# Kernel optimization log

Measured on AMD Instinct MI355X. Metric: run time of the kernel, lower is better.

Reference implementation:

```python
import jax, jax.numpy as jnp
import numpy as np

# --- constants matching DILConfig ---
N_DIFF = 1000      # num_diffusion_steps
STEPS = 4          # inference_steps
S_MAX = 4          # max_scales
BUDGET = 0.2       # entropy_budget
G0 = 2.0           # guidance_strength
ENT_LO = 0.1       # stability_threshold_low
ENT_HI = 0.5       # stability_threshold_high
B, L, C, H = 16, 1024, 128, 512


def setup_inputs() -> dict:
    key = jax.random.key(0)
    ks = jax.random.split(key, 6)
    y_obs = jax.random.normal(ks[0], (B, L, C), dtype=jnp.float32)
    mask = (jax.random.uniform(ks[1], (B, L, C)) > 0.5).astype(jnp.float32)
    z_init = jax.random.normal(ks[2], (B, L, C), dtype=jnp.float32)
    W1 = jax.random.normal(ks[3], (C, H), dtype=jnp.float32) / np.sqrt(C)
    b1 = jnp.zeros((H,), dtype=jnp.float32)
    W2 = jax.random.normal(ks[4], (H, C), dtype=jnp.float32) / np.sqrt(H)
    b2 = jnp.zeros((C,), dtype=jnp.float32)
    tw = jax.random.normal(ks[5], (H,), dtype=jnp.float32)
    return {"y_obs": y_obs, "mask": mask, "z_init": z_init,
            "W1": W1, "b1": b1, "W2": W2, "b2": b2, "tw": tw}


def _dil_forward(y_obs, mask, z_init, W1, b1, W2, b2, tw):
    # diffusion schedule (linear betas)
    betas = jnp.linspace(1e-4, 0.02, N_DIFF, dtype=jnp.float32)
    ac = jnp.cumprod(1.0 - betas)
    alpha = jnp.sqrt(ac)                     # sqrt_alphas_cumprod
    sigma = jnp.sqrt(1.0 - ac)               # sqrt_one_minus_alphas_cumprod
    lam = jnp.log(alpha) - jnp.log(sigma)    # log-SNR/2

    step = N_DIFF // STEPS
    ks = [N_DIFF - 1 - i * step for i in range(STEPS)]

    def score(z, k):
        # epsilon predictor: channel MLP with scalar time feature
        t_feat = jnp.float32(k) / N_DIFF
        h = jax.nn.gelu(jnp.einsum('blc,ch->blh', z, W1) + b1 + t_feat * tw)
        return jnp.einsum('blh,hc->blc', h, W2) + b2

    z = z_init
    for k in ks:  # fixed small unrolled loop over inference steps
        kp = max(k - step, 0)
        eps = score(z, k)                                   # [B,L,C]
        h_lam = lam[kp] - lam[k]
        base_a = alpha[kp] / alpha[k]
        base_b = sigma[kp] * (jnp.exp(h_lam) - 1.0)

        # entropy map: batch-mean |eps| per pixel
        ent_pix = jnp.mean(jnp.abs(eps), axis=0)            # [L,C]

        # self-guidance on observed entries
        obs_err = (z - y_obs) * mask
        guidance = -obs_err / (jnp.var(obs_err) + 1e-8)     # [B,L,C]

        z_new = z
        # coarse -> fine so finer-scale selected nodes overwrite coarser ones
        for s in range(S_MAX - 1, -1, -1):
            w = 2 ** s
            pooled = ent_pix.reshape(L // w, w, C // w, w).mean(axis=(1, 3))
            Knodes = max(1, int(BUDGET * pooled.size))
            _, idx = jax.lax.top_k(pooled.ravel(), Knodes)
            selg = jnp.zeros((pooled.size,), jnp.float32).at[idx].set(1.0)
            selg = selg.reshape(pooled.shape)
            sel = jnp.repeat(jnp.repeat(selg, w, axis=0), w, axis=1)     # [L,C]
            ent_up = jnp.repeat(jnp.repeat(pooled, w, axis=0), w, axis=1)

            # adaptive solver order from entropy stability thresholds
            order = (1.0 + (ent_up > ENT_LO).astype(jnp.float32)
                         + (ent_up > ENT_HI).astype(jnp.float32))
            corr = (1.0 + (order - 1.0) * 0.5 * h_lam
                        + (order - 1.0) * (order - 2.0) / 6.0 * h_lam ** 2)
            gs = G0 * ent_up / (ent_up + 1.0)               # adaptive guidance

            cand = base_a * z - base_b * (corr * eps) + gs * guidance
            z_new = jnp.where(sel[None, :, :] > 0, cand, z_new)
        z = z_new
    return z


def reference(y_obs, mask, z_init, W1, b1, W2, b2, tw):
    return _dil_forward(y_obs, mask, z_init, W1, b1, W2, b2, tw)
```

## Files before the change

kernel.cpp:

```cpp
#include <hip/hip_runtime.h>
#include <math.h>
#include <stdint.h>

#define L_DIM 1024
#define C_DIM 128
#define H_DIM 512
#define B_DIM 16
#define LC (L_DIM * C_DIM)
#define BLC (B_DIM * LC)

typedef __attribute__((ext_vector_type(8))) short short8;
typedef __attribute__((ext_vector_type(4))) float floatx4;

__device__ __forceinline__ unsigned fordbits(unsigned u) {
    return (u & 0x80000000u) ? ~u : (u | 0x80000000u);
}

__device__ __forceinline__ void split3(float x, unsigned& uh, unsigned& um,
                                       unsigned& ul) {
    uh = __float_as_uint(x);
    const float r1 = x - __uint_as_float(uh & 0xffff0000u);
    um = __float_as_uint(r1);
    const float r2 = r1 - __uint_as_float(um & 0xffff0000u);
    ul = __float_as_uint(r2);
}

__device__ __forceinline__ float gelu_fast(float x) {
    const float g = 0.7978845608028654f * (x + 0.044715f * x * x * x);
    const float e = __expf(2.0f * g);
    const float t = 1.0f - 2.0f / (e + 1.0f);
    return 0.5f * x * (1.0f + t);
}

__global__ __launch_bounds__(256) void wsplit_kernel(
    const float* __restrict__ W1, const float* __restrict__ W2,
    unsigned short* __restrict__ W1h, unsigned short* __restrict__ W1m,
    unsigned short* __restrict__ W1l, unsigned short* __restrict__ W2h,
    unsigned short* __restrict__ W2m, unsigned short* __restrict__ W2l,
    unsigned* __restrict__ zeroblk) {
    const int t = blockIdx.x * 256 + threadIdx.x;
    if (t < 16396) zeroblk[t] = 0u;
    unsigned uh, um, ul;
    if (t < 65536) {
        const int j = t & 7, lane = (t >> 3) & 63, nt = (t >> 9) & 31,
                  kt = (t >> 14) & 3;
        const int k = kt * 32 + (lane >> 4) * 8 + j;
        const int n = nt * 16 + (lane & 15);
        split3(W1[k * 512 + n], uh, um, ul);
        W1h[t] = (unsigned short)(uh >> 16);
        W1m[t] = (unsigned short)(um >> 16);
        W1l[t] = (unsigned short)(ul >> 16);
    } else {
        const int t2 = t - 65536;
        const int j = t2 & 7, lane = (t2 >> 3) & 63, nt = (t2 >> 9) & 7,
                  kt = (t2 >> 12) & 15;
        const int k = kt * 32 + (lane >> 4) * 8 + j;
        const int n = nt * 16 + (lane & 15);
        split3(W2[k * 128 + n], uh, um, ul);
        W2h[t2] = (unsigned short)(uh >> 16);
        W2m[t2] = (unsigned short)(um >> 16);
        W2l[t2] = (unsigned short)(ul >> 16);
    }
}

#define MFMA6(AH, AM, AL, BH, BM, BL, ACC)                                    \
    ACC = __builtin_amdgcn_mfma_f32_16x16x32_bf16(AL, BH, ACC, 0, 0, 0);      \
    ACC = __builtin_amdgcn_mfma_f32_16x16x32_bf16(AM, BM, ACC, 0, 0, 0);      \
    ACC = __builtin_amdgcn_mfma_f32_16x16x32_bf16(AH, BL, ACC, 0, 0, 0);      \
    ACC = __builtin_amdgcn_mfma_f32_16x16x32_bf16(AM, BH, ACC, 0, 0, 0);      \
    ACC = __builtin_amdgcn_mfma_f32_16x16x32_bf16(AH, BM, ACC, 0, 0, 0);      \
    ACC = __builtin_amdgcn_mfma_f32_16x16x32_bf16(AH, BH, ACC, 0, 0, 0);

__device__ __forceinline__ int swz(int row, int col) {
    return row * 128 + ((((col >> 3) ^ (row & 15))) << 3) + (col & 7);
}

template <int UPD>
__global__ __launch_bounds__(512, 2) void mlp_kernel(
    float* __restrict__ z, const float* __restrict__ zr,
    const float* __restrict__ y, const float* __restrict__ mk,
    const unsigned short* __restrict__ W1h, const unsigned short* __restrict__ W1m,
    const unsigned short* __restrict__ W1l, const unsigned short* __restrict__ W2h,
    const unsigned short* __restrict__ W2m, const unsigned short* __restrict__ W2l,
    const float* __restrict__ b1, const float* __restrict__ tw,
    const float* __restrict__ b2, float t_feat,
    float* __restrict__ eps_buf, float* __restrict__ ent,
    const float* __restrict__ cA, const float* __restrict__ cB,
    const float* __restrict__ cG, float* __restrict__ accum,
    float* __restrict__ p1, float* __restrict__ p2,
    unsigned* __restrict__ ghist) {
    __shared__ unsigned short zA[3][8192];
    __shared__ unsigned short hA[3][8192];
    __shared__ float entbuf[4][128];
    __shared__ float red1[8], red2[8];
    const int tid = threadIdx.x;
    const int w = tid >> 6, lane = tid & 63;
    const int quad = lane >> 4, m16 = lane & 15;
    const int l0 = blockIdx.x * 4;

    float s1 = 0.f, s2 = 0.f;
#pragma unroll
    for (int e = 0; e < 4; ++e) {
        const int f = (e * 512 + tid) * 4;
        const int r_ = f >> 7, cb = f & 127;
        const int b = r_ & 15, il = r_ >> 4, l = l0 + il;
        const size_t g = ((size_t)b * 1024 + l) * 128 + cb;
        float4 zv = *(const float4*)(zr + g);
        const float4 yv = *(const float4*)(y + g);
        const float4 mv = *(const float4*)(mk + g);
        if (UPD) {
            const float4 ev = *(const float4*)(eps_buf + g);
            const int pix = l * 128 + cb;
            const float4 a4 = *(const float4*)(cA + pix);
            const float4 b4 = *(const float4*)(cB + pix);
            const float4 g4 = *(const float4*)(cG + pix);
            zv.x = a4.x * zv.x - b4.x * ev.x - g4.x * ((zv.x - yv.x) * mv.x);
            zv.y = a4.y * zv.y - b4.y * ev.y - g4.y * ((zv.y - yv.y) * mv.y);
            zv.z = a4.z * zv.z - b4.z * ev.z - g4.z * ((zv.z - yv.z) * mv.z);
            zv.w = a4.w * zv.w - b4.w * ev.w - g4.w * ((zv.w - yv.w) * mv.w);
            *(float4*)(z + g) = zv;
        }
        float oe;
        oe = (zv.x - yv.x) * mv.x; s1 += oe; s2 += oe * oe;
        oe = (zv.y - yv.y) * mv.y; s1 += oe; s2 += oe * oe;
        oe = (zv.z - yv.z) * mv.z; s1 += oe; s2 += oe * oe;
        oe = (zv.w - yv.w) * mv.w; s1 += oe; s2 += oe * oe;

        const int base = swz(r_, cb);
        const float xs[4] = {zv.x, zv.y, zv.z, zv.w};
        ushort4 vh, vm, vl;
        unsigned uh, um, ul;
        split3(xs[0], uh, um, ul); vh.x = uh >> 16; vm.x = um >> 16; vl.x = ul >> 16;
        split3(xs[1], uh, um, ul); vh.y = uh >> 16; vm.y = um >> 16; vl.y = ul >> 16;
        split3(xs[2], uh, um, ul); vh.z = uh >> 16; vm.z = um >> 16; vl.z = ul >> 16;
        split3(xs[3], uh, um, ul); vh.w = uh >> 16; vm.w = um >> 16; vl.w = ul >> 16;
        *(ushort4*)(&zA[0][base]) = vh;
        *(ushort4*)(&zA[1][base]) = vm;
        *(ushort4*)(&zA[2][base]) = vl;
    }
#pragma unroll
    for (int off = 32; off; off >>= 1) {
        s1 += __shfl_down(s1, off);
        s2 += __shfl_down(s2, off);
    }
    if (lane == 0) { red1[w] = s1; red2[w] = s2; }
    __syncthreads();
    if (tid == 0) {
        float a1 = 0.f, a2 = 0.f;
#pragma unroll
        for (int i = 0; i < 8; ++i) { a1 += red1[i]; a2 += red2[i]; }
        atomicAdd(&accum[0], a1);
        atomicAdd(&accum[1], a2);
    }

    floatx4 acc1[16];
#pragma unroll
    for (int i = 0; i < 16; ++i) acc1[i] = (floatx4){0.f, 0.f, 0.f, 0.f};

#pragma unroll
    for (int kt = 0; kt < 4; ++kt) {
        short8 Ah[4], Am[4], Al[4];
#pragma unroll
        for (int il = 0; il < 4; ++il) {
            const int fb = swz(il * 16 + m16, kt * 32 + quad * 8);
            Ah[il] = *(const short8*)(&zA[0][fb]);
            Am[il] = *(const short8*)(&zA[1][fb]);
            Al[il] = *(const short8*)(&zA[2][fb]);
        }
#pragma unroll
        for (int q = 0; q < 4; ++q) {
            const size_t off = ((size_t)(kt * 32 + q * 8 + w) * 64 + lane) * 8;
            const short8 bh = *(const short8*)(W1h + off);
            const short8 bm = *(const short8*)(W1m + off);
            const short8 bl = *(const short8*)(W1l + off);
#pragma unroll
            for (int il = 0; il < 4; ++il) {
                floatx4 a = acc1[q * 4 + il];
                MFMA6(Ah[il], Am[il], Al[il], bh, bm, bl, a);
                acc1[q * 4 + il] = a;
            }
        }
    }

    floatx4 acc2[4];
#pragma unroll
    for (int i = 0; i < 4; ++i) acc2[i] = (floatx4){0.f, 0.f, 0.f, 0.f};

#pragma unroll
    for (int q = 0; q < 4; ++q) {
        {
            const int colg = q * 128 + w * 16 + m16;
            const float bb = b1[colg] + t_feat * tw[colg];
            const int kcol = w * 16 + m16;
#pragma unroll
            for (int il = 0; il < 4; ++il) {
#pragma unroll
                for (int r = 0; r < 4; ++r) {
                    const float x = gelu_fast(acc1[q * 4 + il][r] + bb);
                    unsigned uh, um, ul;
                    split3(x, uh, um, ul);
                    const int idx = swz(il * 16 + quad * 4 + r, kcol);
                    hA[0][idx] = (unsigned short)(uh >> 16);
                    hA[1][idx] = (unsigned short)(um >> 16);
                    hA[2][idx] = (unsigned short)(ul >> 16);
                }
            }
        }
        __syncthreads();

#pragma unroll
        for (int ktl = 0; ktl < 4; ++ktl) {
            short8 Ah2[4], Am2[4], Al2[4];
#pragma unroll
            for (int il = 0; il < 4; ++il) {
                const int fb = swz(il * 16 + m16, ktl * 32 + quad * 8);
                Ah2[il] = *(const short8*)(&hA[0][fb]);
                Am2[il] = *(const short8*)(&hA[1][fb]);
                Al2[il] = *(const short8*)(&hA[2][fb]);
            }
            const size_t off =
                ((size_t)((q * 4 + ktl) * 8 + w) * 64 + lane) * 8;
            const short8 bh = *(const short8*)(W2h + off);
            const short8 bm = *(const short8*)(W2m + off);
            const short8 bl = *(const short8*)(W2l + off);
#pragma unroll
            for (int il = 0; il < 4; ++il) {
                floatx4 a = acc2[il];
                MFMA6(Ah2[il], Am2[il], Al2[il], bh, bm, bl, a);
                acc2[il] = a;
            }
        }
        __syncthreads();
    }

    {
        const int col = w * 16 + m16;
        const float bb2 = b2[col];
#pragma unroll
        for (int il = 0; il < 4; ++il) {
            float pa = 0.f;
#pragma unroll
            for (int r = 0; r < 4; ++r) {
                const float e = acc2[il][r] + bb2;
                const int b = quad * 4 + r;
                eps_buf[((size_t)b * 1024 + l0 + il) * 128 + col] = e;
                pa += fabsf(e);
            }
            pa += __shfl_xor(pa, 16);
            pa += __shfl_xor(pa, 32);
            if (quad == 0) {
                const float ev = pa * (1.0f / 16.0f);
                ent[(l0 + il) * 128 + col] = ev;
                entbuf[il][col] = ev;
            }
        }
    }

    unsigned* lhist = (unsigned*)&hA[0][0];
    for (int i = tid; i < 8192; i += 512) lhist[i] = 0u;
    __syncthreads();
    if (tid < 512) {
        const float v = entbuf[tid >> 7][tid & 127];
        const unsigned b = fordbits(__float_as_uint(v)) >> 18;
        atomicAdd(&lhist[b >> 1], 1u << ((b & 1) << 4));
    }
    if (tid < 128) {
        const int ir = tid >> 6, c = tid & 63;
        float s = entbuf[2 * ir][2 * c];
        s += entbuf[2 * ir][2 * c + 1];
        s += entbuf[2 * ir + 1][2 * c];
        s += entbuf[2 * ir + 1][2 * c + 1];
        p1[(2 * (int)blockIdx.x + ir) * 64 + c] = s * 0.25f;
    }
    if (tid < 32) {
        const int c = tid;
        float s = 0.f;
#pragma unroll
        for (int ii = 0; ii < 4; ++ii) {
            s += entbuf[ii][4 * c];
            s += entbuf[ii][4 * c + 1];
            s += entbuf[ii][4 * c + 2];
            s += entbuf[ii][4 * c + 3];
        }
        p2[(int)blockIdx.x * 32 + c] = s * 0.0625f;
    }
    __syncthreads();
    for (int i = tid; i < 8192; i += 512) {
        const unsigned v = lhist[i];
        if (v & 0xFFFFu) atomicAdd(&ghist[2 * i], v & 0xFFFFu);
        if (v >> 16) atomicAdd(&ghist[2 * i + 1], v >> 16);
    }
}


__device__ __forceinline__ void suffix_scan_block(unsigned* __restrict__ part,
                                                  unsigned* __restrict__ wtot,
                                                  const int n, const int t) {
    const int lane = t & 63, w = t >> 6;
    const int nw = n >> 6;
    unsigned s = (t < n) ? part[t] : 0u;
#pragma unroll
    for (int off = 1; off < 64; off <<= 1) {
        const unsigned v = __shfl_down(s, off);
        if (lane + off < 64) s += v;
    }
    if (t < n && lane == 0) wtot[w] = s;
    __syncthreads();
    if (t < n) {
        unsigned o = 0;
        for (int j = w + 1; j < nw; ++j) o += wtot[j];
        part[t] = s + o;
    }
    __syncthreads();
}

#define CAND_CAP 16384

__device__ __forceinline__ void wave_compact(bool pred, unsigned val,
                                             unsigned* __restrict__ sh_cnt,
                                             unsigned* __restrict__ buf,
                                             const int lane) {
    const unsigned long long mask = __ballot(pred);
    if (mask == 0ull) return;
    unsigned base = 0u;
    if (lane == 0)
        base = atomicAdd(sh_cnt, (unsigned)__popcll(mask));
    base = __shfl(base, 0);
    if (pred) {
        const unsigned rank =
            (unsigned)__popcll(mask & ((1ull << lane) - 1ull));
        const unsigned p = base + rank;
        if (p < CAND_CAP) buf[p] = val;
    }
}

template <int NPT4, int N, unsigned K>
__device__ __forceinline__ void small_select_vals(
    const float4* xv, unsigned* __restrict__ gout, const int t,
    const int w8, unsigned* __restrict__ histcand,
    unsigned* __restrict__ part, unsigned (*hrep)[512],
    unsigned* __restrict__ wtot,
    unsigned* sh_b, unsigned* sh_krem, unsigned* sh_cnt, unsigned* sh_d,
    unsigned* sh_k2) {
    const int lane = t & 63;
    unsigned u[NPT4 * 4];
#pragma unroll
    for (int i = 0; i < NPT4; ++i) {
        u[4 * i + 0] = fordbits(__float_as_uint(xv[i].x));
        u[4 * i + 1] = fordbits(__float_as_uint(xv[i].y));
        u[4 * i + 2] = fordbits(__float_as_uint(xv[i].z));
        u[4 * i + 3] = fordbits(__float_as_uint(xv[i].w));
    }
    if (t == 0) { *sh_b = 0u; *sh_krem = 1u; *sh_cnt = 0u; *sh_d = 0u; *sh_k2 = 1u; }
    for (int i = t; i < 16384; i += 1024) histcand[i] = 0u;
    __syncthreads();
#pragma unroll
    for (int j = 0; j < NPT4 * 4; ++j) atomicAdd(&histcand[u[j] >> 18], 1u);
    __syncthreads();
    {
        unsigned s = 0;
#pragma unroll
        for (int j = 0; j < 16; ++j) s += histcand[t * 16 + j];
        part[t] = s;
    }
    suffix_scan_block(part, wtot, 1024, t);
    {
        const unsigned suf = part[t];
        const unsigned sufn = (t < 1023) ? part[t + 1] : 0u;
        if (suf >= K && sufn < K) {
            unsigned run = sufn;
            for (int b = 15; b >= 0; --b) {
                const unsigned hb = histcand[t * 16 + b];
                run += hb;
                if (run >= K) {
                    *sh_b = (unsigned)(t * 16 + b);
                    *sh_krem = K - (run - hb);
                    break;
                }
            }
        }
    }
    __syncthreads();
    const unsigned b14 = *sh_b;
    unsigned krem = *sh_krem;
    __syncthreads();
#pragma unroll
    for (int j = 0; j < NPT4 * 4; ++j)
        wave_compact((u[j] >> 18) == b14, u[j], sh_cnt, histcand, lane);
    __syncthreads();
    const unsigned cnt = *sh_cnt;
    const bool inlds = (cnt <= CAND_CAP);
    for (int i = t; i < 4096; i += 1024) ((unsigned*)hrep)[i] = 0u;
    __syncthreads();
    if (inlds) {
        for (unsigned i = t; i < cnt; i += 1024)
            atomicAdd(&hrep[w8][(histcand[i] >> 9) & 511u], 1u);
    } else {
#pragma unroll
        for (int j = 0; j < NPT4 * 4; ++j)
            if ((u[j] >> 18) == b14)
                atomicAdd(&hrep[w8][(u[j] >> 9) & 511u], 1u);
    }
    __syncthreads();
    if (t < 512) {
        unsigned s = 0;
#pragma unroll
        for (int r = 0; r < 8; ++r) s += hrep[r][t];
        part[t] = s;
    }
    __syncthreads();
    suffix_scan_block(part, wtot, 512, t);
    if (t < 512) {
        const unsigned suf = part[t];
        const unsigned sufn = (t < 511) ? part[t + 1] : 0u;
        if (suf >= krem && sufn < krem) { *sh_d = (unsigned)t; *sh_k2 = krem - sufn; }
    }
    __syncthreads();
    const unsigned dA = *sh_d;
    krem = *sh_k2;
    __syncthreads();
    for (int i = t; i < 4096; i += 1024) ((unsigned*)hrep)[i] = 0u;
    __syncthreads();
    if (inlds) {
        for (unsigned i = t; i < cnt; i += 1024) {
            const unsigned c = histcand[i];
            if (((c >> 9) & 511u) == dA) atomicAdd(&hrep[w8][c & 511u], 1u);
        }
    } else {
#pragma unroll
        for (int j = 0; j < NPT4 * 4; ++j)
            if ((u[j] >> 18) == b14 && ((u[j] >> 9) & 511u) == dA)
                atomicAdd(&hrep[w8][u[j] & 511u], 1u);
    }
    __syncthreads();
    if (t < 512) {
        unsigned s = 0;
#pragma unroll
        for (int r = 0; r < 8; ++r) s += hrep[r][t];
        part[t] = s;
    }
    __syncthreads();
    suffix_scan_block(part, wtot, 512, t);
    if (t < 512) {
        const unsigned suf = part[t];
        const unsigned sufn = (t < 511) ? part[t + 1] : 0u;
        if (suf >= krem && sufn < krem)
            gout[0] = (b14 << 18) | (dA << 9) | (unsigned)t;
    }
}

__global__ __launch_bounds__(1024, 1) void thresh_kernel(
    const float* __restrict__ ent, const float* __restrict__ p1,
    const float* __restrict__ p2, float* __restrict__ p3,
    const unsigned* __restrict__ ghist, unsigned* __restrict__ gprefix) {
    const int scale = blockIdx.x, t = threadIdx.x;
    __shared__ unsigned histcand[16384];
    __shared__ unsigned part[1024];
    __shared__ unsigned hrep[8][512];
    __shared__ unsigned wtot[16];
    __shared__ unsigned sh_b, sh_krem, sh_cnt, sh_d, sh_k2;
    const int w8 = (t >> 6) & 7;
    const int lane = t & 63;

    if (scale == 1) {
        float4 xv[8];
#pragma unroll
        for (int i = 0; i < 8; ++i) xv[i] = ((const float4*)p1)[t + i * 1024];
        small_select_vals<8, 32768, 6553u>(xv, &gprefix[1], t, w8, histcand,
                                           part, hrep, wtot, &sh_b, &sh_krem,
                                           &sh_cnt, &sh_d, &sh_k2);
        return;
    }
    if (scale == 2) {
        float4 xv[2];
#pragma unroll
        for (int i = 0; i < 2; ++i) xv[i] = ((const float4*)p2)[t + i * 1024];
        small_select_vals<2, 8192, 1638u>(xv, &gprefix[2], t, w8, histcand,
                                          part, hrep, wtot, &sh_b, &sh_krem,
                                          &sh_cnt, &sh_d, &sh_k2);
        return;
    }
    if (scale == 3) {
        float4 xv[1];
        if (t < 512) {
            float sv[4];
#pragma unroll
            for (int jdx = 0; jdx < 4; ++jdx) {
                const int e = t * 4 + jdx;
                const int r = e >> 4, c = e & 15;
                float s = 0.f;
#pragma unroll
                for (int ii = 0; ii < 8; ++ii) {
                    const float4 ea =
                        *(const float4*)(ent + (((r * 8 + ii) << 7) + c * 8));
                    const float4 eb =
                        *(const float4*)(ent + (((r * 8 + ii) << 7) + c * 8 + 4));
                    s += ea.x; s += ea.y; s += ea.z; s += ea.w;
                    s += eb.x; s += eb.y; s += eb.z; s += eb.w;
                }
                sv[jdx] = s * (1.0f / 64.0f);
            }
            xv[0] = (float4){sv[0], sv[1], sv[2], sv[3]};
            *(float4*)(p3 + t * 4) = xv[0];
        } else {
            xv[0] = (float4){-1e30f, -1e30f, -1e30f, -1e30f};
        }
        small_select_vals<1, 2048, 409u>(xv, &gprefix[3], t, w8, histcand,
                                         part, hrep, wtot, &sh_b, &sh_krem,
                                         &sh_cnt, &sh_d, &sh_k2);
        return;
    }

    const unsigned K = 26214u;
    if (t == 0) { sh_b = 0u; sh_krem = 1u; sh_cnt = 0u; sh_d = 0u; sh_k2 = 1u; }

    {
        unsigned s = 0;
        const uint4* h4 = (const uint4*)(ghist + t * 16);
#pragma unroll
        for (int j = 0; j < 4; ++j) {
            const uint4 x = h4[j];
            s += x.x + x.y + x.z + x.w;
        }
        part[t] = s;
    }
    __syncthreads();
    suffix_scan_block(part, wtot, 1024, t);
    {
        const unsigned suf = part[t];
        const unsigned sufn = (t < 1023) ? part[t + 1] : 0u;
        if (suf >= K && sufn < K) {
            unsigned run = sufn;
            for (int b = 15; b >= 0; --b) {
                const unsigned hb = ghist[t * 16 + b];
                run += hb;
                if (run >= K) {
                    sh_b = (unsigned)(t * 16 + b);
                    sh_krem = K - (run - hb);
                    break;
                }
            }
        }
    }
    __syncthreads();
    const unsigned b14 = sh_b;
    unsigned krem = sh_krem;

    for (int base = 0; base < 32768; base += 8192) {
        float4 w4[8];
#pragma unroll
        for (int i = 0; i < 8; ++i)
            w4[i] = ((const float4*)ent)[base + i * 1024 + t];
#pragma unroll
        for (int i = 0; i < 8; ++i) {
            const float xs[4] = {w4[i].x, w4[i].y, w4[i].z, w4[i].w};
#pragma unroll
            for (int j = 0; j < 4; ++j) {
                const unsigned uu = fordbits(__float_as_uint(xs[j]));
                wave_compact((uu >> 18) == b14, uu, &sh_cnt, histcand, lane);
            }
        }
    }
    __syncthreads();
    const unsigned cnt = sh_cnt;
    const bool inlds = (cnt <= CAND_CAP);

    for (int i = t; i < 4096; i += 1024) ((unsigned*)hrep)[i] = 0u;
    __syncthreads();
    if (inlds) {
        for (unsigned i = t; i < cnt; i += 1024)
            atomicAdd(&hrep[w8][(histcand[i] >> 9) & 511u], 1u);
    } else {
        for (int base = 0; base < 32768; base += 8192) {
            float4 w4[8];
#pragma unroll
            for (int i = 0; i < 8; ++i)
                w4[i] = ((const float4*)ent)[base + i * 1024 + t];
#pragma unroll
            for (int i = 0; i < 8; ++i) {
                const float xs[4] = {w4[i].x, w4[i].y, w4[i].z, w4[i].w};
#pragma unroll
                for (int j = 0; j < 4; ++j) {
                    const unsigned uu = fordbits(__float_as_uint(xs[j]));
                    if ((uu >> 18) == b14)
                        atomicAdd(&hrep[w8][(uu >> 9) & 511u], 1u);
                }
            }
        }
    }
    __syncthreads();
    if (t < 512) {
        unsigned s = 0;
#pragma unroll
        for (int r = 0; r < 8; ++r) s += hrep[r][t];
        part[t] = s;
    }
    __syncthreads();
    suffix_scan_block(part, wtot, 512, t);
    if (t < 512) {
        const unsigned suf = part[t];
        const unsigned sufn = (t < 511) ? part[t + 1] : 0u;
        if (suf >= krem && sufn < krem) { sh_d = (unsigned)t; sh_k2 = krem - sufn; }
    }
    __syncthreads();
    const unsigned dA = sh_d;
    krem = sh_k2;
    __syncthreads();

    for (int i = t; i < 4096; i += 1024) ((unsigned*)hrep)[i] = 0u;
    __syncthreads();
    if (inlds) {
        for (unsigned i = t; i < cnt; i += 1024) {
            const unsigned c = histcand[i];
            if (((c >> 9) & 511u) == dA) atomicAdd(&hrep[w8][c & 511u], 1u);
        }
    } else {
        for (int base = 0; base < 32768; base += 8192) {
            float4 w4[8];
#pragma unroll
            for (int i = 0; i < 8; ++i)
                w4[i] = ((const float4*)ent)[base + i * 1024 + t];
#pragma unroll
            for (int i = 0; i < 8; ++i) {
                const float xs[4] = {w4[i].x, w4[i].y, w4[i].z, w4[i].w};
#pragma unroll
                for (int j = 0; j < 4; ++j) {
                    const unsigned uu = fordbits(__float_as_uint(xs[j]));
                    if ((uu >> 18) == b14 && ((uu >> 9) & 511u) == dA)
                        atomicAdd(&hrep[w8][uu & 511u], 1u);
                }
            }
        }
    }
    __syncthreads();
    if (t < 512) {
        unsigned s = 0;
#pragma unroll
        for (int r = 0; r < 8; ++r) s += hrep[r][t];
        part[t] = s;
    }
    __syncthreads();
    suffix_scan_block(part, wtot, 512, t);
    if (t < 512) {
        const unsigned suf = part[t];
        const unsigned sufn = (t < 511) ? part[t + 1] : 0u;
        if (suf >= krem && sufn < krem)
            gprefix[0] = (b14 << 18) | (dA << 9) | (unsigned)t;
    }
}

__global__ __launch_bounds__(256) void coeff_kernel(
    const float* __restrict__ ent, const float* __restrict__ p1,
    const float* __restrict__ p2, const float* __restrict__ p3,
    const unsigned* __restrict__ gprefix, const float* __restrict__ accum_si,
    float* __restrict__ cA, float* __restrict__ cB, float* __restrict__ cG,
    unsigned* __restrict__ ghist, float base_a, float base_b, float h_lam) {
    const int i = blockIdx.x * 256 + threadIdx.x;
    if (i < 16384) ghist[i] = 0u;

    const unsigned t0 = gprefix[0], t1 = gprefix[1], t2 = gprefix[2],
                   t3 = gprefix[3];
    const float mean = accum_si[0] * (1.0f / (float)BLC);
    const float var = accum_si[1] * (1.0f / (float)BLC) - mean * mean;
    const float vinv = 1.0f / (var + 1e-8f);

    const int l = i >> 7, c = i & 127;
    float ent_v = 0.f;
    bool sel = false;
    const float v0 = ent[i];
    if (fordbits(__float_as_uint(v0)) >= t0) { ent_v = v0; sel = true; }
    else {
        const float v1 = p1[((l >> 1) << 6) + (c >> 1)];
        if (fordbits(__float_as_uint(v1)) >= t1) { ent_v = v1; sel = true; }
        else {
            const float v2 = p2[((l >> 2) << 5) + (c >> 2)];
            if (fordbits(__float_as_uint(v2)) >= t2) { ent_v = v2; sel = true; }
            else {
                const float v3 = p3[((l >> 3) << 4) + (c >> 3)];
                if (fordbits(__float_as_uint(v3)) >= t3) { ent_v = v3; sel = true; }
            }
        }
    }
    if (sel) {
        float corr;
        if (ent_v > 0.5f)
            corr = 1.0f + h_lam + h_lam * h_lam * (1.0f / 3.0f);
        else if (ent_v > 0.1f)
            corr = 1.0f + 0.5f * h_lam;
        else
            corr = 1.0f;
        cA[i] = base_a;
        cB[i] = base_b * corr;
        cG[i] = (2.0f * ent_v / (ent_v + 1.0f)) * vinv;
    } else {
        cA[i] = 1.0f;
        cB[i] = 0.f;
        cG[i] = 0.f;
    }
}

__global__ __launch_bounds__(256) void update_kernel(
    float* __restrict__ z, const float* __restrict__ y,
    const float* __restrict__ mk, const float* __restrict__ eps,
    const float* __restrict__ cA, const float* __restrict__ cB,
    const float* __restrict__ cG) {
    const int idx = blockIdx.x * 256 + threadIdx.x;
    const int p = idx & (LC - 1);
    const float zi = z[idx];
    z[idx] = cA[p] * zi - cB[p] * eps[idx] - cG[p] * ((zi - y[idx]) * mk[idx]);
}

extern "C" void kernel_launch(void* const* d_in, const int* in_sizes, int n_in,
                              void* d_out, int out_size, void* d_ws,
                              size_t ws_size, hipStream_t stream) {
    const float* y_obs = (const float*)d_in[0];
    const float* mask = (const float*)d_in[1];
    const float* z_init = (const float*)d_in[2];
    const float* W1 = (const float*)d_in[3];
    const float* b1 = (const float*)d_in[4];
    const float* W2 = (const float*)d_in[5];
    const float* b2 = (const float*)d_in[6];
    const float* tw = (const float*)d_in[7];
    float* z = (float*)d_out;
    float* ws = (float*)d_ws;

    float* eps = ws;
    float* ent = ws + 2097152;
    float* p1 = ws + 2228224;
    float* p2 = ws + 2260992;
    float* p3 = ws + 2269184;
    float* cA = ws + 2271232;
    float* cB = ws + 2402304;
    float* cG = ws + 2533376;
    float* accum = ws + 2664448;
    unsigned* gprefix = (unsigned*)(ws + 2664456);
    unsigned* ghist = (unsigned*)(ws + 2664460);
    unsigned short* W1h = (unsigned short*)(ws + 2680844);
    unsigned short* W1m = (unsigned short*)(ws + 2713612);
    unsigned short* W1l = (unsigned short*)(ws + 2746380);
    unsigned short* W2h = (unsigned short*)(ws + 2779148);
    unsigned short* W2m = (unsigned short*)(ws + 2811916);
    unsigned short* W2l = (unsigned short*)(ws + 2844684);

    float alpha_[1000], sigma_[1000], lam_[1000];
    {
        float ac = 1.0f;
        for (int i = 0; i < 1000; ++i) {
            const float beta = 1e-4f + (0.02f - 1e-4f) * ((float)i / 999.0f);
            ac = ac * (1.0f - beta);
            alpha_[i] = sqrtf(ac);
            sigma_[i] = sqrtf(1.0f - ac);
            lam_[i] = logf(alpha_[i]) - logf(sigma_[i]);
        }
    }
    float tf[4], hl[4], ba[4], bb[4];
    for (int si = 0; si < 4; ++si) {
        const int k = 999 - si * 250;
        const int kp = (k - 250 > 0) ? (k - 250) : 0;
        tf[si] = (float)k / 1000.0f;
        hl[si] = lam_[kp] - lam_[k];
        ba[si] = alpha_[kp] / alpha_[k];
        bb[si] = sigma_[kp] * (expf(hl[si]) - 1.0f);
    }

    wsplit_kernel<<<512, 256, 0, stream>>>(W1, W2, W1h, W1m, W1l, W2h, W2m,
                                           W2l, (unsigned*)accum);

    for (int si = 0; si < 4; ++si) {
        const float* zrd = (si <= 1) ? z_init : z;
        if (si == 0) {
            mlp_kernel<0><<<256, 512, 0, stream>>>(
                z, zrd, y_obs, mask, W1h, W1m, W1l, W2h, W2m, W2l, b1, tw, b2,
                tf[0], eps, ent, cA, cB, cG, accum, p1, p2, ghist);
        } else {
            mlp_kernel<1><<<256, 512, 0, stream>>>(
                z, zrd, y_obs, mask, W1h, W1m, W1l, W2h, W2m, W2l, b1, tw, b2,
                tf[si], eps, ent, cA, cB, cG, accum + 2 * si, p1, p2, ghist);
        }
        thresh_kernel<<<4, 1024, 0, stream>>>(ent, p1, p2, p3, ghist, gprefix);
        coeff_kernel<<<512, 256, 0, stream>>>(ent, p1, p2, p3, gprefix,
                                              accum + 2 * si, cA, cB, cG,
                                              ghist, ba[si], bb[si], hl[si]);
    }
    update_kernel<<<8192, 256, 0, stream>>>(z, y_obs, mask, eps, cA, cB, cG);
}
```

Before: 381.3 us.

## Fuse per-step coefficient computation into MLP prologue and simplify entropy histogram

```diff
diff --git a/kernel.cpp b/kernel.cpp
--- a/kernel.cpp
+++ b/kernel.cpp
@@ -85,18 +85,57 @@
     const float* __restrict__ b1, const float* __restrict__ tw,
     const float* __restrict__ b2, float t_feat,
     float* __restrict__ eps_buf, float* __restrict__ ent,
-    const float* __restrict__ cA, const float* __restrict__ cB,
-    const float* __restrict__ cG, float* __restrict__ accum,
     float* __restrict__ p1, float* __restrict__ p2,
-    unsigned* __restrict__ ghist) {
+    const float* __restrict__ p3, const unsigned* __restrict__ gprefix,
+    const float* __restrict__ accum_prev, float* __restrict__ accum_cur,
+    unsigned* __restrict__ ghist, float base_a, float base_b, float h_lam) {
     __shared__ unsigned short zA[3][8192];
     __shared__ unsigned short hA[3][8192];
-    __shared__ float entbuf[4][128];
+    __shared__ float cfA[512], cfB[512], cfG[512];
     __shared__ float red1[8], red2[8];
     const int tid = threadIdx.x;
     const int w = tid >> 6, lane = tid & 63;
     const int quad = lane >> 4, m16 = lane & 15;
-    const int l0 = blockIdx.x * 4;
+    const int bid = (int)blockIdx.x;
+    const int l0 = bid * 4;
+
+    if (UPD) {
+        const int il = tid >> 7, c = tid & 127;
+        const int l = l0 + il;
+        const int pix = l * 128 + c;
+        const float v0 = ent[pix];
+        const float v1 = p1[((l >> 1) << 6) + (c >> 1)];
+        const float v2 = p2[((l >> 2) << 5) + (c >> 2)];
+        const float v3 = p3[((l >> 3) << 4) + (c >> 3)];
+        const unsigned t0 = gprefix[0], t1 = gprefix[1], t2 = gprefix[2],
+                       t3 = gprefix[3];
+        const float mean = accum_prev[0] * (1.0f / (float)BLC);
+        const float var = accum_prev[1] * (1.0f / (float)BLC) - mean * mean;
+        const float vinv = 1.0f / (var + 1e-8f);
+        float ent_v = 0.f;
+        bool sel = false;
+        if (fordbits(__float_as_uint(v0)) >= t0) { ent_v = v0; sel = true; }
+        else if (fordbits(__float_as_uint(v1)) >= t1) { ent_v = v1; sel = true; }
+        else if (fordbits(__float_as_uint(v2)) >= t2) { ent_v = v2; sel = true; }
+        else if (fordbits(__float_as_uint(v3)) >= t3) { ent_v = v3; sel = true; }
+        float ca, cb_, cg;
+        if (sel) {
+            float corr;
+            if (ent_v > 0.5f)
+                corr = 1.0f + h_lam + h_lam * h_lam * (1.0f / 3.0f);
+            else if (ent_v > 0.1f)
+                corr = 1.0f + 0.5f * h_lam;
+            else
+                corr = 1.0f;
+            ca = base_a;
+            cb_ = base_b * corr;
+            cg = (2.0f * ent_v / (ent_v + 1.0f)) * vinv;
+        } else {
+            ca = 1.0f; cb_ = 0.f; cg = 0.f;
+        }
+        cfA[tid] = ca; cfB[tid] = cb_; cfG[tid] = cg;
+        __syncthreads();
+    }
 
     float s1 = 0.f, s2 = 0.f;
 #pragma unroll
@@ -110,10 +149,10 @@
         const float4 mv = *(const float4*)(mk + g);
         if (UPD) {
             const float4 ev = *(const float4*)(eps_buf + g);
-            const int pix = l * 128 + cb;
-            const float4 a4 = *(const float4*)(cA + pix);
-            const float4 b4 = *(const float4*)(cB + pix);
-            const float4 g4 = *(const float4*)(cG + pix);
+            const int ci = il * 128 + cb;
+            const float4 a4 = *(const float4*)(&cfA[ci]);
+            const float4 b4 = *(const float4*)(&cfB[ci]);
+            const float4 g4 = *(const float4*)(&cfG[ci]);
             zv.x = a4.x * zv.x - b4.x * ev.x - g4.x * ((zv.x - yv.x) * mv.x);
             zv.y = a4.y * zv.y - b4.y * ev.y - g4.y * ((zv.y - yv.y) * mv.y);
             zv.z = a4.z * zv.z - b4.z * ev.z - g4.z * ((zv.z - yv.z) * mv.z);
@@ -149,8 +188,8 @@
         float a1 = 0.f, a2 = 0.f;
 #pragma unroll
         for (int i = 0; i < 8; ++i) { a1 += red1[i]; a2 += red2[i]; }
-        atomicAdd(&accum[0], a1);
-        atomicAdd(&accum[1], a2);
+        atomicAdd(&accum_cur[0], a1);
+        atomicAdd(&accum_cur[1], a2);
     }
 
     floatx4 acc1[16];
@@ -236,6 +275,7 @@
     {
         const int col = w * 16 + m16;
         const float bb2 = b2[col];
+        float ev[4];
 #pragma unroll
         for (int il = 0; il < 4; ++il) {
             float pa = 0.f;
@@ -248,47 +288,35 @@
             }
             pa += __shfl_xor(pa, 16);
             pa += __shfl_xor(pa, 32);
-            if (quad == 0) {
-                const float ev = pa * (1.0f / 16.0f);
-                ent[(l0 + il) * 128 + col] = ev;
-                entbuf[il][col] = ev;
-            }
-        }
-    }
-
-    unsigned* lhist = (unsigned*)&hA[0][0];
-    for (int i = tid; i < 8192; i += 512) lhist[i] = 0u;
-    __syncthreads();
-    if (tid < 512) {
-        const float v = entbuf[tid >> 7][tid & 127];
-        const unsigned b = fordbits(__float_as_uint(v)) >> 18;
-        atomicAdd(&lhist[b >> 1], 1u << ((b & 1) << 4));
-    }
-    if (tid < 128) {
-        const int ir = tid >> 6, c = tid & 63;
-        float s = entbuf[2 * ir][2 * c];
-        s += entbuf[2 * ir][2 * c + 1];
-        s += entbuf[2 * ir + 1][2 * c];
-        s += entbuf[2 * ir + 1][2 * c + 1];
-        p1[(2 * (int)blockIdx.x + ir) * 64 + c] = s * 0.25f;
-    }
-    if (tid < 32) {
-        const int c = tid;
-        float s = 0.f;
-#pragma unroll
-        for (int ii = 0; ii < 4; ++ii) {
-            s += entbuf[ii][4 * c];
-            s += entbuf[ii][4 * c + 1];
-            s += entbuf[ii][4 * c + 2];
-            s += entbuf[ii][4 * c + 3];
-        }
-        p2[(int)blockIdx.x * 32 + c] = s * 0.0625f;
-    }
-    __syncthreads();
-    for (int i = tid; i < 8192; i += 512) {
-        const unsigned v = lhist[i];
-        if (v & 0xFFFFu) atomicAdd(&ghist[2 * i], v & 0xFFFFu);
-        if (v >> 16) atomicAdd(&ghist[2 * i + 1], v >> 16);
+            ev[il] = pa * (1.0f / 16.0f);
+        }
+        if (quad == 0) {
+#pragma unroll
+            for (int il = 0; il < 4; ++il) {
+                ent[(l0 + il) * 128 + col] = ev[il];
+                atomicAdd(&ghist[fordbits(__float_as_uint(ev[il])) >> 18], 1u);
+            }
+        }
+        float c1[4];
+#pragma unroll
+        for (int il = 0; il < 4; ++il) c1[il] = __shfl(ev[il], lane | 1);
+#pragma unroll
+        for (int ir = 0; ir < 2; ++ir) {
+            float s = ev[2 * ir];
+            s += c1[2 * ir];
+            s += ev[2 * ir + 1];
+            s += c1[2 * ir + 1];
+            if (quad == 0 && !(m16 & 1))
+                p1[(2 * bid + ir) * 64 + w * 8 + (m16 >> 1)] = s * 0.25f;
+        }
+        float s2 = 0.f;
+#pragma unroll
+        for (int ii = 0; ii < 4; ++ii)
+#pragma unroll
+            for (int j = 0; j < 4; ++j)
+                s2 += __shfl(ev[ii], (lane & ~3) | j);
+        if (quad == 0 && !(m16 & 3))
+            p2[bid * 32 + w * 4 + (m16 >> 2)] = s2 * 0.0625f;
     }
 }
 
@@ -452,7 +480,7 @@
 __global__ __launch_bounds__(1024, 1) void thresh_kernel(
     const float* __restrict__ ent, const float* __restrict__ p1,
     const float* __restrict__ p2, float* __restrict__ p3,
-    const unsigned* __restrict__ ghist, unsigned* __restrict__ gprefix) {
+    unsigned* __restrict__ ghist, unsigned* __restrict__ gprefix) {
     const int scale = blockIdx.x, t = threadIdx.x;
     __shared__ unsigned histcand[16384];
     __shared__ unsigned part[1024];
@@ -546,6 +574,8 @@
     const unsigned b14 = sh_b;
     unsigned krem = sh_krem;
 
+    for (int i = t; i < 16384; i += 1024) ghist[i] = 0u;
+
     for (int base = 0; base < 32768; base += 8192) {
         float4 w4[8];
 #pragma unroll
@@ -654,9 +684,8 @@
     const float* __restrict__ p2, const float* __restrict__ p3,
     const unsigned* __restrict__ gprefix, const float* __restrict__ accum_si,
     float* __restrict__ cA, float* __restrict__ cB, float* __restrict__ cG,
-    unsigned* __restrict__ ghist, float base_a, float base_b, float h_lam) {
+    float base_a, float base_b, float h_lam) {
     const int i = blockIdx.x * 256 + threadIdx.x;
-    if (i < 16384) ghist[i] = 0u;
 
     const unsigned t0 = gprefix[0], t1 = gprefix[1], t2 = gprefix[2],
                    t3 = gprefix[3];
@@ -771,16 +800,17 @@
         if (si == 0) {
             mlp_kernel<0><<<256, 512, 0, stream>>>(
                 z, zrd, y_obs, mask, W1h, W1m, W1l, W2h, W2m, W2l, b1, tw, b2,
-                tf[0], eps, ent, cA, cB, cG, accum, p1, p2, ghist);
+                tf[0], eps, ent, p1, p2, p3, gprefix, accum, accum, ghist,
+                0.f, 0.f, 0.f);
         } else {
             mlp_kernel<1><<<256, 512, 0, stream>>>(
                 z, zrd, y_obs, mask, W1h, W1m, W1l, W2h, W2m, W2l, b1, tw, b2,
-                tf[si], eps, ent, cA, cB, cG, accum + 2 * si, p1, p2, ghist);
+                tf[si], eps, ent, p1, p2, p3, gprefix, accum + 2 * (si - 1),
+                accum + 2 * si, ghist, ba[si - 1], bb[si - 1], hl[si - 1]);
         }
         thresh_kernel<<<4, 1024, 0, stream>>>(ent, p1, p2, p3, ghist, gprefix);
-        coeff_kernel<<<512, 256, 0, stream>>>(ent, p1, p2, p3, gprefix,
-                                              accum + 2 * si, cA, cB, cG,
-                                              ghist, ba[si], bb[si], hl[si]);
-    }
+    }
+    coeff_kernel<<<512, 256, 0, stream>>>(ent, p1, p2, p3, gprefix, accum + 6,
+                                          cA, cB, cG, ba[3], bb[3], hl[3]);
     update_kernel<<<8192, 256, 0, stream>>>(z, y_obs, mask, eps, cA, cB, cG);
 }
```

New measurement: 1.111 ms. 2.91x slower.
